# Performance work log

Hardware: AMD Instinct MI355X
Metric: run time of the kernel (lower is better)

The kernel has to match this reference:

```python
import jax, jax.numpy as jnp
import numpy as np

B, L, T = 256, 256, 50  # batch, max_len, num_tags


def setup_inputs() -> dict:
    key = jax.random.key(0)
    k1, k2, k3 = jax.random.split(key, 3)
    feats = jax.random.normal(k1, (B, L, T), dtype=jnp.float32)
    trans_m = jax.random.normal(k2, (T, T), dtype=jnp.float32)
    tags = jax.random.randint(k3, (B, L), 0, T)
    mask = jnp.ones((B, L), dtype=jnp.int32)
    return {"feats": feats, "trans_m": trans_m, "tags": tags, "mask": mask}


def _normalizer(logits, trans_m, m):
    # logits: (L, B, T), m: (L, B) float mask
    alpha0 = logits[0]  # (B, T)

    def step(alpha, inp):
        emit, mt = inp  # (B, T), (B,)
        # (B, T_from, T_to) broadcast add, logsumexp over T_from
        tmp = alpha[:, :, None] + trans_m[None, :, :] + emit[:, None, :]
        new = jax.nn.logsumexp(tmp, axis=1)
        alpha = jnp.where(mt[:, None] > 0, new, alpha)
        return alpha, None

    alpha, _ = jax.lax.scan(step, alpha0, (logits[1:], m[1:]))
    return jax.nn.logsumexp(alpha, axis=1)  # (B,)


def _gold_score(logits, trans_m, tags_t, m):
    # logits: (L, B, T); tags_t: (L, B); m: (L, B)
    trans_sc = trans_m[tags_t[:-1], tags_t[1:]] * m[1:]  # (L-1, B)
    emit_sc = jnp.take_along_axis(logits, tags_t[:, :, None], axis=2)[..., 0] * m  # (L, B)
    return jnp.sum(trans_sc + emit_sc[:-1], axis=0) + emit_sc[-1]  # (B,)


def reference(feats, trans_m, tags, mask):
    # feats: (B, L, T) -> (L, B, T); include_start_end_trans=False
    logits = jnp.transpose(feats, (1, 0, 2))
    tags_t = tags.T
    m = mask.T.astype(feats.dtype)
    all_path = _normalizer(logits, trans_m, m)
    gold = _gold_score(logits, trans_m, tags_t, m)
    return all_path - gold  # (B,) loss per example
```

## Files before the change

kernel.cpp:

```cpp
#include <hip/hip_runtime.h>
#include <math.h>


#define TAGS 50
#define LEN 256
#define NB 256
#define HALF 128
#define INV_LN2 1.4426950408889634f
#define LN2 0.6931471805599453f

typedef __attribute__((ext_vector_type(8))) short bf16x8;
typedef __attribute__((ext_vector_type(4))) float f32x4;

#if __has_builtin(__builtin_amdgcn_exp2f)
#define EXP2F(x) __builtin_amdgcn_exp2f(x)
#else
#define EXP2F(x) exp2f(x)
#endif
#if __has_builtin(__builtin_amdgcn_logf)
#define LOG2F(x) __builtin_amdgcn_logf(x)
#else
#define LOG2F(x) log2f(x)
#endif
#if __has_builtin(__builtin_amdgcn_rcpf)
#define RCPF(x) __builtin_amdgcn_rcpf(x)
#else
#define RCPF(x) (1.0f / (x))
#endif

__device__ __forceinline__ float readlane_f(float v, int srclane) {
  return __builtin_bit_cast(float,
      __builtin_amdgcn_readlane(__builtin_bit_cast(int, v), srclane));
}

__device__ __forceinline__ int bf16pair(float lo, float hi) {
  unsigned lb = (__builtin_bit_cast(unsigned, lo) + 0x8000u) >> 16;
  unsigned hb = (__builtin_bit_cast(unsigned, hi) + 0x8000u) & 0xFFFF0000u;
  return (int)(hb | lb);
}

union U8 { int i[4]; bf16x8 v; };

#define WS_U(b)  ((b) * 64)
#define WS_W(b)  ((NB + (b)) * 64)
#define WS_SF(b) (2 * NB * 64 + (b))
#define WS_SB(b) (2 * NB * 64 + NB + (b))

__global__ __launch_bounds__(64) void crf_scan_kernel(
    const float* __restrict__ feats,
    const float* __restrict__ trans,
    const int*   __restrict__ mask,
    float*       __restrict__ ws)
{
  const int bid    = blockIdx.x;
  const bool is_fwd = bid < NB;
  const int b      = is_fwd ? bid : bid - NB;
  const int lane   = threadIdx.x;
  const int q      = lane >> 4;
  const int n      = lane & 15;

  __shared__ __align__(16) float fl[HALF * TAGS];
  __shared__ int ml[HALF];

  const int base_l = is_fwd ? 0 : HALF;
  const float* fb = feats + ((size_t)b * LEN + base_l) * TAGS;
  const int*   mb = mask + b * LEN + base_l;

  {
    const float4* fv = (const float4*)fb;
    for (int i = lane; i < (HALF * TAGS) / 4; i += 64) {
      float4 v4 = fv[i];
      v4.x *= INV_LN2; v4.y *= INV_LN2; v4.z *= INV_LN2; v4.w *= INV_LN2;
      *(float4*)&fl[i * 4] = v4;
    }
    for (int i = lane; i < HALF; i += 64) ml[i] = mb[i];
  }

  int tcl[4], vld[4];
#pragma unroll
  for (int t = 0; t < 4; ++t) {
    const int tg = n + 16 * t;
    vld[t] = tg < TAGS;
    tcl[t] = vld[t] ? tg : (TAGS - 1);
  }

  U8 Bfr[4][2];
#pragma unroll
  for (int t = 0; t < 4; ++t)
#pragma unroll
    for (int c = 0; c < 2; ++c)
#pragma unroll
      for (int r = 0; r < 4; ++r) {
        const int col = 16 * t + n;
        const int tag0 = 16 * c + 4 * q + r;
        const int tag1 = tag0 + 32;
        float e0 = 0.0f, e1 = 0.0f;
        if (col < TAGS) {
          if (tag0 < TAGS)
            e0 = EXP2F((is_fwd ? trans[tag0 * TAGS + col]
                               : trans[col * TAGS + tag0]) * INV_LN2);
          if (tag1 < TAGS)
            e1 = EXP2F((is_fwd ? trans[tag1 * TAGS + col]
                               : trans[col * TAGS + tag1]) * INV_LN2);
        }
        Bfr[t][c].i[r] = bf16pair(e0, e1);
      }

  int addr[4];
#pragma unroll
  for (int r = 0; r < 4; ++r) addr[r] = (4 * q + r) * 4;

  __syncthreads();

  const f32x4 zero4 = {0.0f, 0.0f, 0.0f, 0.0f};
  float v[4], S;

  if (is_fwd) {
    const float c0 = fl[0];
#pragma unroll
    for (int t = 0; t < 4; ++t) v[t] = vld[t] ? EXP2F(fl[tcl[t]] - c0) : 0.0f;
    S = c0;

    float eh[4];
#pragma unroll
    for (int t = 0; t < 4; ++t) eh[t] = EXP2F(fl[TAGS + tcl[t]]);
    int m_nxt = ml[1];

    for (int l = 1; l < HALF; ++l) {
      const int m_cur = m_nxt;
      const int ln = (l + 1 < HALF) ? (l + 1) : (HALF - 1);

      const int P0 = bf16pair(v[0], v[2]);
      const int P1 = bf16pair(v[1], v[3]);
      const float cc = readlane_f(v[0], 0);
      const float rr = RCPF(cc);

      U8 A0, A1;
#pragma unroll
      for (int r = 0; r < 4; ++r) {
        A0.i[r] = __builtin_amdgcn_ds_bpermute(addr[r], P0);
        A1.i[r] = __builtin_amdgcn_ds_bpermute(addr[r], P1);
      }

      f32x4 d0 = __builtin_amdgcn_mfma_f32_16x16x32_bf16(A0.v, Bfr[0][0].v, zero4, 0, 0, 0);
      f32x4 d1 = __builtin_amdgcn_mfma_f32_16x16x32_bf16(A0.v, Bfr[1][0].v, zero4, 0, 0, 0);
      f32x4 d2 = __builtin_amdgcn_mfma_f32_16x16x32_bf16(A0.v, Bfr[2][0].v, zero4, 0, 0, 0);
      f32x4 d3 = __builtin_amdgcn_mfma_f32_16x16x32_bf16(A0.v, Bfr[3][0].v, zero4, 0, 0, 0);
      f32x4 g0 = __builtin_amdgcn_mfma_f32_16x16x32_bf16(A1.v, Bfr[0][1].v, zero4, 0, 0, 0);
      f32x4 g1 = __builtin_amdgcn_mfma_f32_16x16x32_bf16(A1.v, Bfr[1][1].v, zero4, 0, 0, 0);
      f32x4 g2 = __builtin_amdgcn_mfma_f32_16x16x32_bf16(A1.v, Bfr[2][1].v, zero4, 0, 0, 0);
      f32x4 g3 = __builtin_amdgcn_mfma_f32_16x16x32_bf16(A1.v, Bfr[3][1].v, zero4, 0, 0, 0);

      float ehn[4];
#pragma unroll
      for (int t = 0; t < 4; ++t) ehn[t] = fl[ln * TAGS + tcl[t]];
      const int m_n2 = ml[ln];

      v[0] = ((m_cur > 0) ? (d0[0] + g0[0]) * eh[0] : v[0]) * rr;
      v[1] = ((m_cur > 0) ? (d1[0] + g1[0]) * eh[1] : v[1]) * rr;
      v[2] = ((m_cur > 0) ? (d2[0] + g2[0]) * eh[2] : v[2]) * rr;
      v[3] = ((m_cur > 0) ? (d3[0] + g3[0]) * eh[3] : v[3]) * rr;
      S += LOG2F(cc);
#pragma unroll
      for (int t = 0; t < 4; ++t) eh[t] = EXP2F(ehn[t]);
      m_nxt = m_n2;
    }

    if (lane < 16) {
#pragma unroll
      for (int t = 0; t < 4; ++t) ws[WS_U(b) + n + 16 * t] = v[t];
    }
    if (lane == 0) ws[WS_SF(b)] = S;
  } else {
#pragma unroll
    for (int t = 0; t < 4; ++t) v[t] = vld[t] ? 1.0f : 0.0f;
    S = 0.0f;

    float eh[4];
#pragma unroll
    for (int t = 0; t < 4; ++t) eh[t] = EXP2F(fl[(HALF - 1) * TAGS + tcl[t]]);
    int m_nxt = ml[HALF - 1];

    for (int l = HALF - 1; l >= 0; --l) {
      const int m_cur = m_nxt;
      const int ln = (l > 0) ? (l - 1) : 0;

      const float x0 = v[0] * eh[0];
      const float x1 = v[1] * eh[1];
      const float x2 = v[2] * eh[2];
      const float x3 = v[3] * eh[3];
      const int P0 = bf16pair(x0, x2);
      const int P1 = bf16pair(x1, x3);
      const float cc = readlane_f(v[0], 0);
      const float rr = RCPF(cc);

      U8 A0, A1;
#pragma unroll
      for (int r = 0; r < 4; ++r) {
        A0.i[r] = __builtin_amdgcn_ds_bpermute(addr[r], P0);
        A1.i[r] = __builtin_amdgcn_ds_bpermute(addr[r], P1);
      }

      f32x4 d0 = __builtin_amdgcn_mfma_f32_16x16x32_bf16(A0.v, Bfr[0][0].v, zero4, 0, 0, 0);
      f32x4 d1 = __builtin_amdgcn_mfma_f32_16x16x32_bf16(A0.v, Bfr[1][0].v, zero4, 0, 0, 0);
      f32x4 d2 = __builtin_amdgcn_mfma_f32_16x16x32_bf16(A0.v, Bfr[2][0].v, zero4, 0, 0, 0);
      f32x4 d3 = __builtin_amdgcn_mfma_f32_16x16x32_bf16(A0.v, Bfr[3][0].v, zero4, 0, 0, 0);
      f32x4 g0 = __builtin_amdgcn_mfma_f32_16x16x32_bf16(A1.v, Bfr[0][1].v, zero4, 0, 0, 0);
      f32x4 g1 = __builtin_amdgcn_mfma_f32_16x16x32_bf16(A1.v, Bfr[1][1].v, zero4, 0, 0, 0);
      f32x4 g2 = __builtin_amdgcn_mfma_f32_16x16x32_bf16(A1.v, Bfr[2][1].v, zero4, 0, 0, 0);
      f32x4 g3 = __builtin_amdgcn_mfma_f32_16x16x32_bf16(A1.v, Bfr[3][1].v, zero4, 0, 0, 0);

      float ehn[4];
#pragma unroll
      for (int t = 0; t < 4; ++t) ehn[t] = fl[ln * TAGS + tcl[t]];
      const int m_n2 = ml[ln];

      v[0] = ((m_cur > 0) ? (d0[0] + g0[0]) : v[0]) * rr;
      v[1] = ((m_cur > 0) ? (d1[0] + g1[0]) : v[1]) * rr;
      v[2] = ((m_cur > 0) ? (d2[0] + g2[0]) : v[2]) * rr;
      v[3] = ((m_cur > 0) ? (d3[0] + g3[0]) : v[3]) * rr;
      S += LOG2F(cc);
#pragma unroll
      for (int t = 0; t < 4; ++t) eh[t] = EXP2F(ehn[t]);
      m_nxt = m_n2;
    }

    if (lane < 16) {
#pragma unroll
      for (int t = 0; t < 4; ++t) ws[WS_W(b) + n + 16 * t] = v[t];
    }
    if (lane == 0) ws[WS_SB(b)] = S;
  }
}

__global__ __launch_bounds__(64) void crf_combine_kernel(
    const float* __restrict__ feats,
    const float* __restrict__ trans,
    const int*   __restrict__ tags,
    const int*   __restrict__ mask,
    const float* __restrict__ ws,
    float*       __restrict__ out)
{
  const int b = blockIdx.x;
  const int lane = threadIdx.x;

  float s = ws[WS_U(b) + lane] * ws[WS_W(b) + lane];
#pragma unroll
  for (int off = 32; off; off >>= 1) s += __shfl_xor(s, off, 64);

  const float* fb = feats + (size_t)b * (LEN * TAGS);
  const int*   tb = tags + b * LEN;
  const int*   mb = mask + b * LEN;
  float gp = 0.0f;
#pragma unroll
  for (int k = 0; k < 4; ++k) {
    const int p = lane + 64 * k;
    const int tg = tb[p];
    if (mb[p] > 0) {
      float vv = fb[p * TAGS + tg];
      if (p >= 1) vv += trans[tb[p - 1] * TAGS + tg];
      gp += vv;
    }
  }
#pragma unroll
  for (int off = 32; off; off >>= 1) gp += __shfl_xor(gp, off, 64);

  if (lane == 0) {
    const float Sf = ws[WS_SF(b)];
    const float Sb = ws[WS_SB(b)];
    out[b] = LN2 * (Sf + Sb + LOG2F(s)) - gp;
  }
}

extern "C" void kernel_launch(void* const* d_in, const int* in_sizes, int n_in,
                              void* d_out, int out_size, void* d_ws, size_t ws_size,
                              hipStream_t stream) {
  const float* feats = (const float*)d_in[0];
  const float* trans = (const float*)d_in[1];
  const int*   tags  = (const int*)d_in[2];
  const int*   mask  = (const int*)d_in[3];
  float* out = (float*)d_out;
  float* ws  = (float*)d_ws;

  crf_scan_kernel<<<2 * NB, 64, 0, stream>>>(feats, trans, mask, ws);
  crf_combine_kernel<<<NB, 64, 0, stream>>>(feats, trans, tags, mask, ws, out);
}
```

Measured before the change: 102.5 us.

## Swap MFMA operand roles to drop per-step bpermute shuffles and precompute emission exps

The transition matrix now sits in the A operand and the alpha vector in the B operand, so the MFMA output lands in the layout needed for the next step's input. This removes the eight ds_bpermute cross-lane shuffles on the serial recurrence path, at the cost of each lane holding 16 state values and doing more pack/multiply work. Emission exponentials are computed once into a padded shared buffer before the loop, replacing per-step exp2 calls with vector LDS loads. The two half-K MFMAs are chained through the accumulator instead of being summed separately, and the loop is unrolled by two.

After: 116.8 us. 14.0% more time.

```diff
diff --git a/kernel.cpp b/kernel.cpp
--- a/kernel.cpp
+++ b/kernel.cpp
@@ -59,7 +59,8 @@
   const int q      = lane >> 4;
   const int n      = lane & 15;
 
-  __shared__ __align__(16) float fl[HALF * TAGS];
+  __shared__ __align__(16) float fraw[HALF * TAGS];
+  __shared__ __align__(16) float flexp[HALF * 64];
   __shared__ int ml[HALF];
 
   const int base_l = is_fwd ? 0 : HALF;
@@ -71,20 +72,20 @@
     for (int i = lane; i < (HALF * TAGS) / 4; i += 64) {
       float4 v4 = fv[i];
       v4.x *= INV_LN2; v4.y *= INV_LN2; v4.z *= INV_LN2; v4.w *= INV_LN2;
-      *(float4*)&fl[i * 4] = v4;
+      *(float4*)&fraw[i * 4] = v4;
     }
     for (int i = lane; i < HALF; i += 64) ml[i] = mb[i];
   }
-
-  int tcl[4], vld[4];
-#pragma unroll
-  for (int t = 0; t < 4; ++t) {
-    const int tg = n + 16 * t;
-    vld[t] = tg < TAGS;
-    tcl[t] = vld[t] ? tg : (TAGS - 1);
-  }
-
-  U8 Bfr[4][2];
+  __syncthreads();
+
+  for (int l = 0; l < HALF; ++l) {
+    float v = 0.0f;
+    if (lane < TAGS) v = EXP2F(fraw[l * TAGS + lane]);
+    flexp[l * 64 + lane] = v;
+  }
+  __syncthreads();
+
+  U8 Afr[4][2];
 #pragma unroll
   for (int t = 0; t < 4; ++t)
 #pragma unroll
@@ -103,134 +104,150 @@
             e1 = EXP2F((is_fwd ? trans[tag1 * TAGS + col]
                                : trans[col * TAGS + tag1]) * INV_LN2);
         }
-        Bfr[t][c].i[r] = bf16pair(e0, e1);
-      }
-
-  int addr[4];
-#pragma unroll
-  for (int r = 0; r < 4; ++r) addr[r] = (4 * q + r) * 4;
-
-  __syncthreads();
+        Afr[t][c].i[r] = bf16pair(e0, e1);
+      }
 
   const f32x4 zero4 = {0.0f, 0.0f, 0.0f, 0.0f};
-  float v[4], S;
+
+#define LDEH(l_, I_) (*(const f32x4*)&flexp[(l_) * 64 + 16 * (I_) + 4 * q])
+
+  float va[16];
+  float S;
 
   if (is_fwd) {
-    const float c0 = fl[0];
-#pragma unroll
-    for (int t = 0; t < 4; ++t) v[t] = vld[t] ? EXP2F(fl[tcl[t]] - c0) : 0.0f;
-    S = c0;
-
-    float eh[4];
-#pragma unroll
-    for (int t = 0; t < 4; ++t) eh[t] = EXP2F(fl[TAGS + tcl[t]]);
+    const float r0 = RCPF(flexp[0]);
+    {
+      f32x4 i0 = LDEH(0, 0), i1 = LDEH(0, 1), i2 = LDEH(0, 2), i3 = LDEH(0, 3);
+#pragma unroll
+      for (int r = 0; r < 4; ++r) {
+        va[r]      = i0[r] * r0;
+        va[4 + r]  = i1[r] * r0;
+        va[8 + r]  = i2[r] * r0;
+        va[12 + r] = i3[r] * r0;
+      }
+    }
+    S = fraw[0];
+
+    f32x4 eh0 = LDEH(1, 0), eh1 = LDEH(1, 1), eh2 = LDEH(1, 2), eh3 = LDEH(1, 3);
     int m_nxt = ml[1];
 
+#pragma unroll 2
     for (int l = 1; l < HALF; ++l) {
       const int m_cur = m_nxt;
       const int ln = (l + 1 < HALF) ? (l + 1) : (HALF - 1);
 
-      const int P0 = bf16pair(v[0], v[2]);
-      const int P1 = bf16pair(v[1], v[3]);
-      const float cc = readlane_f(v[0], 0);
+      const float cc = readlane_f(va[0], 0);
       const float rr = RCPF(cc);
 
-      U8 A0, A1;
-#pragma unroll
-      for (int r = 0; r < 4; ++r) {
-        A0.i[r] = __builtin_amdgcn_ds_bpermute(addr[r], P0);
-        A1.i[r] = __builtin_amdgcn_ds_bpermute(addr[r], P1);
-      }
-
-      f32x4 d0 = __builtin_amdgcn_mfma_f32_16x16x32_bf16(A0.v, Bfr[0][0].v, zero4, 0, 0, 0);
-      f32x4 d1 = __builtin_amdgcn_mfma_f32_16x16x32_bf16(A0.v, Bfr[1][0].v, zero4, 0, 0, 0);
-      f32x4 d2 = __builtin_amdgcn_mfma_f32_16x16x32_bf16(A0.v, Bfr[2][0].v, zero4, 0, 0, 0);
-      f32x4 d3 = __builtin_amdgcn_mfma_f32_16x16x32_bf16(A0.v, Bfr[3][0].v, zero4, 0, 0, 0);
-      f32x4 g0 = __builtin_amdgcn_mfma_f32_16x16x32_bf16(A1.v, Bfr[0][1].v, zero4, 0, 0, 0);
-      f32x4 g1 = __builtin_amdgcn_mfma_f32_16x16x32_bf16(A1.v, Bfr[1][1].v, zero4, 0, 0, 0);
-      f32x4 g2 = __builtin_amdgcn_mfma_f32_16x16x32_bf16(A1.v, Bfr[2][1].v, zero4, 0, 0, 0);
-      f32x4 g3 = __builtin_amdgcn_mfma_f32_16x16x32_bf16(A1.v, Bfr[3][1].v, zero4, 0, 0, 0);
-
-      float ehn[4];
-#pragma unroll
-      for (int t = 0; t < 4; ++t) ehn[t] = fl[ln * TAGS + tcl[t]];
+      U8 B0, B1;
+#pragma unroll
+      for (int r = 0; r < 4; ++r) {
+        B0.i[r] = bf16pair(va[r],     va[8 + r]);
+        B1.i[r] = bf16pair(va[4 + r], va[12 + r]);
+      }
+
+      f32x4 d0 = __builtin_amdgcn_mfma_f32_16x16x32_bf16(Afr[0][1].v, B1.v, zero4, 0, 0, 0);
+      f32x4 d1 = __builtin_amdgcn_mfma_f32_16x16x32_bf16(Afr[1][1].v, B1.v, zero4, 0, 0, 0);
+      f32x4 d2 = __builtin_amdgcn_mfma_f32_16x16x32_bf16(Afr[2][1].v, B1.v, zero4, 0, 0, 0);
+      f32x4 d3 = __builtin_amdgcn_mfma_f32_16x16x32_bf16(Afr[3][1].v, B1.v, zero4, 0, 0, 0);
+      d0 = __builtin_amdgcn_mfma_f32_16x16x32_bf16(Afr[0][0].v, B0.v, d0, 0, 0, 0);
+      d1 = __builtin_amdgcn_mfma_f32_16x16x32_bf16(Afr[1][0].v, B0.v, d1, 0, 0, 0);
+      d2 = __builtin_amdgcn_mfma_f32_16x16x32_bf16(Afr[2][0].v, B0.v, d2, 0, 0, 0);
+      d3 = __builtin_amdgcn_mfma_f32_16x16x32_bf16(Afr[3][0].v, B0.v, d3, 0, 0, 0);
+
+      f32x4 en0 = LDEH(ln, 0), en1 = LDEH(ln, 1), en2 = LDEH(ln, 2), en3 = LDEH(ln, 3);
       const int m_n2 = ml[ln];
 
-      v[0] = ((m_cur > 0) ? (d0[0] + g0[0]) * eh[0] : v[0]) * rr;
-      v[1] = ((m_cur > 0) ? (d1[0] + g1[0]) * eh[1] : v[1]) * rr;
-      v[2] = ((m_cur > 0) ? (d2[0] + g2[0]) * eh[2] : v[2]) * rr;
-      v[3] = ((m_cur > 0) ? (d3[0] + g3[0]) * eh[3] : v[3]) * rr;
+#pragma unroll
+      for (int r = 0; r < 4; ++r) {
+        va[r]      = ((m_cur > 0) ? d0[r] * eh0[r] : va[r])      * rr;
+        va[4 + r]  = ((m_cur > 0) ? d1[r] * eh1[r] : va[4 + r])  * rr;
+        va[8 + r]  = ((m_cur > 0) ? d2[r] * eh2[r] : va[8 + r])  * rr;
+        va[12 + r] = ((m_cur > 0) ? d3[r] * eh3[r] : va[12 + r]) * rr;
+      }
       S += LOG2F(cc);
-#pragma unroll
-      for (int t = 0; t < 4; ++t) eh[t] = EXP2F(ehn[t]);
+      eh0 = en0; eh1 = en1; eh2 = en2; eh3 = en3;
       m_nxt = m_n2;
     }
 
-    if (lane < 16) {
-#pragma unroll
-      for (int t = 0; t < 4; ++t) ws[WS_U(b) + n + 16 * t] = v[t];
+    if (n == 0) {
+#pragma unroll
+      for (int I = 0; I < 4; ++I)
+#pragma unroll
+        for (int r = 0; r < 4; ++r)
+          ws[WS_U(b) + 16 * I + 4 * q + r] = va[4 * I + r];
     }
     if (lane == 0) ws[WS_SF(b)] = S;
   } else {
 #pragma unroll
-    for (int t = 0; t < 4; ++t) v[t] = vld[t] ? 1.0f : 0.0f;
+    for (int I = 0; I < 4; ++I)
+#pragma unroll
+      for (int r = 0; r < 4; ++r)
+        va[4 * I + r] = (16 * I + 4 * q + r < TAGS) ? 1.0f : 0.0f;
     S = 0.0f;
 
-    float eh[4];
-#pragma unroll
-    for (int t = 0; t < 4; ++t) eh[t] = EXP2F(fl[(HALF - 1) * TAGS + tcl[t]]);
+    f32x4 eh0 = LDEH(HALF - 1, 0), eh1 = LDEH(HALF - 1, 1),
+          eh2 = LDEH(HALF - 1, 2), eh3 = LDEH(HALF - 1, 3);
     int m_nxt = ml[HALF - 1];
 
+#pragma unroll 2
     for (int l = HALF - 1; l >= 0; --l) {
       const int m_cur = m_nxt;
       const int ln = (l > 0) ? (l - 1) : 0;
 
-      const float x0 = v[0] * eh[0];
-      const float x1 = v[1] * eh[1];
-      const float x2 = v[2] * eh[2];
-      const float x3 = v[3] * eh[3];
-      const int P0 = bf16pair(x0, x2);
-      const int P1 = bf16pair(x1, x3);
-      const float cc = readlane_f(v[0], 0);
+      const float cc = readlane_f(va[0], 0);
       const float rr = RCPF(cc);
 
-      U8 A0, A1;
-#pragma unroll
-      for (int r = 0; r < 4; ++r) {
-        A0.i[r] = __builtin_amdgcn_ds_bpermute(addr[r], P0);
-        A1.i[r] = __builtin_amdgcn_ds_bpermute(addr[r], P1);
-      }
-
-      f32x4 d0 = __builtin_amdgcn_mfma_f32_16x16x32_bf16(A0.v, Bfr[0][0].v, zero4, 0, 0, 0);
-      f32x4 d1 = __builtin_amdgcn_mfma_f32_16x16x32_bf16(A0.v, Bfr[1][0].v, zero4, 0, 0, 0);
-      f32x4 d2 = __builtin_amdgcn_mfma_f32_16x16x32_bf16(A0.v, Bfr[2][0].v, zero4, 0, 0, 0);
-      f32x4 d3 = __builtin_amdgcn_mfma_f32_16x16x32_bf16(A0.v, Bfr[3][0].v, zero4, 0, 0, 0);
-      f32x4 g0 = __builtin_amdgcn_mfma_f32_16x16x32_bf16(A1.v, Bfr[0][1].v, zero4, 0, 0, 0);
-      f32x4 g1 = __builtin_amdgcn_mfma_f32_16x16x32_bf16(A1.v, Bfr[1][1].v, zero4, 0, 0, 0);
-      f32x4 g2 = __builtin_amdgcn_mfma_f32_16x16x32_bf16(A1.v, Bfr[2][1].v, zero4, 0, 0, 0);
-      f32x4 g3 = __builtin_amdgcn_mfma_f32_16x16x32_bf16(A1.v, Bfr[3][1].v, zero4, 0, 0, 0);
-
-      float ehn[4];
-#pragma unroll
-      for (int t = 0; t < 4; ++t) ehn[t] = fl[ln * TAGS + tcl[t]];
+      float x[16];
+#pragma unroll
+      for (int r = 0; r < 4; ++r) {
+        x[r]      = va[r]      * eh0[r];
+        x[4 + r]  = va[4 + r]  * eh1[r];
+        x[8 + r]  = va[8 + r]  * eh2[r];
+        x[12 + r] = va[12 + r] * eh3[r];
+      }
+
+      U8 B0, B1;
+#pragma unroll
+      for (int r = 0; r < 4; ++r) {
+        B0.i[r] = bf16pair(x[r],     x[8 + r]);
+        B1.i[r] = bf16pair(x[4 + r], x[12 + r]);
+      }
+
+      f32x4 d0 = __builtin_amdgcn_mfma_f32_16x16x32_bf16(Afr[0][1].v, B1.v, zero4, 0, 0, 0);
+      f32x4 d1 = __builtin_amdgcn_mfma_f32_16x16x32_bf16(Afr[1][1].v, B1.v, zero4, 0, 0, 0);
+      f32x4 d2 = __builtin_amdgcn_mfma_f32_16x16x32_bf16(Afr[2][1].v, B1.v, zero4, 0, 0, 0);
+      f32x4 d3 = __builtin_amdgcn_mfma_f32_16x16x32_bf16(Afr[3][1].v, B1.v, zero4, 0, 0, 0);
+      d0 = __builtin_amdgcn_mfma_f32_16x16x32_bf16(Afr[0][0].v, B0.v, d0, 0, 0, 0);
+      d1 = __builtin_amdgcn_mfma_f32_16x16x32_bf16(Afr[1][0].v, B0.v, d1, 0, 0, 0);
+      d2 = __builtin_amdgcn_mfma_f32_16x16x32_bf16(Afr[2][0].v, B0.v, d2, 0, 0, 0);
+      d3 = __builtin_amdgcn_mfma_f32_16x16x32_bf16(Afr[3][0].v, B0.v, d3, 0, 0, 0);
+
+      f32x4 en0 = LDEH(ln, 0), en1 = LDEH(ln, 1), en2 = LDEH(ln, 2), en3 = LDEH(ln, 3);
       const int m_n2 = ml[ln];
 
-      v[0] = ((m_cur > 0) ? (d0[0] + g0[0]) : v[0]) * rr;
-      v[1] = ((m_cur > 0) ? (d1[0] + g1[0]) : v[1]) * rr;
-      v[2] = ((m_cur > 0) ? (d2[0] + g2[0]) : v[2]) * rr;
-      v[3] = ((m_cur > 0) ? (d3[0] + g3[0]) : v[3]) * rr;
+#pragma unroll
+      for (int r = 0; r < 4; ++r) {
+        va[r]      = ((m_cur > 0) ? d0[r] : va[r])      * rr;
+        va[4 + r]  = ((m_cur > 0) ? d1[r] : va[4 + r])  * rr;
+        va[8 + r]  = ((m_cur > 0) ? d2[r] : va[8 + r])  * rr;
+        va[12 + r] = ((m_cur > 0) ? d3[r] : va[12 + r]) * rr;
+      }
       S += LOG2F(cc);
-#pragma unroll
-      for (int t = 0; t < 4; ++t) eh[t] = EXP2F(ehn[t]);
+      eh0 = en0; eh1 = en1; eh2 = en2; eh3 = en3;
       m_nxt = m_n2;
     }
 
-    if (lane < 16) {
-#pragma unroll
-      for (int t = 0; t < 4; ++t) ws[WS_W(b) + n + 16 * t] = v[t];
+    if (n == 0) {
+#pragma unroll
+      for (int I = 0; I < 4; ++I)
+#pragma unroll
+        for (int r = 0; r < 4; ++r)
+          ws[WS_W(b) + 16 * I + 4 * q + r] = va[4 * I + r];
     }
     if (lane == 0) ws[WS_SB(b)] = S;
   }
+#undef LDEH
 }
 
 __global__ __launch_bounds__(64) void crf_combine_kernel(
```
